# Kernel tuning notes

Measured on AMD Instinct MI355X. Metric: run time of the kernel, lower is better.

The kernel has to match this reference:

```python
import jax, jax.numpy as jnp
import numpy as np


def _pairwise_sqdist(a, b):
    # a: [m, n, d], b: [m, n, d] -> M: [m, n, n], M[m,i,j] = ||a[m,i]-b[m,j]||^2
    # Use the expansion |a|^2 + |b|^2 - 2 a.b to avoid materializing the
    # [m, n, n, d] difference tensor; clamp tiny negatives from cancellation.
    a2 = jnp.sum(a * a, axis=-1)  # [m, n]
    b2 = jnp.sum(b * b, axis=-1)  # [m, n]
    ab = jnp.einsum('mid,mjd->mij', a, b)  # [m, n, n]
    return jnp.maximum(a2[:, :, None] + b2[:, None, :] - 2.0 * ab, 0.0)


def setup_inputs() -> dict:
    key = jax.random.key(0)
    k1, k2 = jax.random.split(key)
    template = jax.random.normal(k1, (16, 4096, 3), dtype=jnp.float32)
    source = jax.random.normal(k2, (16, 4096, 3), dtype=jnp.float32)
    return {"template": template, "source": source}


def reference(template, source):
    M = _pairwise_sqdist(template, source)  # [m, n, n]
    # min over template index (axis 1): nearest template point for each source point
    dist1 = jnp.mean(jnp.sqrt(jnp.min(M, axis=1)))
    # min over source index (axis 2): nearest source point for each template point
    dist2 = jnp.mean(jnp.sqrt(jnp.min(M, axis=2)))
    return (dist1 + dist2) / 2.0
```

## Files before the change

### kernel.cpp

```cpp
#include <hip/hip_runtime.h>

#define N_PTS   4096
#define N_BATCH 16
#define INV_CNT (1.0f / (2.0f * N_BATCH * N_PTS))
#define AROW_BYTES ((size_t)2 * N_BATCH * N_PTS * 16 * 2)
#define NBLK    512

typedef _Float16 f16x8  __attribute__((ext_vector_type(8)));

__global__ __launch_bounds__(256) void prep_kernel(
    const float* __restrict__ tpl, const float* __restrict__ src,
    _Float16* __restrict__ arow, float* __restrict__ out) {
    int pt = blockIdx.x * 256 + threadIdx.x;
    if (pt == 0) out[0] = 0.0f;
    const float* p = (pt < 65536 ? tpl : src) + (size_t)(pt & 65535) * 3;
    float x = p[0], y = p[1], z = p[2];
    float o2 = fmaf(x, x, fmaf(y, y, z * z));
    _Float16 xh = (_Float16)x, yh = (_Float16)y, zh = (_Float16)z;
    _Float16 xl = (_Float16)(x - (float)xh);
    _Float16 yl = (_Float16)(y - (float)yh);
    _Float16 zl = (_Float16)(z - (float)zh);
    _Float16 o2h = (_Float16)o2;
    _Float16 o2l = (_Float16)(o2 - (float)o2h);
    const _Float16 m2 = (_Float16)-2.0f;
    f16x8 v0, v1;
    v0[0] = m2 * xh; v0[1] = m2 * yh; v0[2] = m2 * zh;
    v0[3] = m2 * xl; v0[4] = m2 * yl; v0[5] = m2 * zl;
    v0[6] = m2 * xh; v0[7] = m2 * yh;
    v1[0] = m2 * zh; v1[1] = o2h; v1[2] = o2l;
    v1[3] = (_Float16)0.0f; v1[4] = (_Float16)0.0f; v1[5] = (_Float16)0.0f;
    v1[6] = (_Float16)0.0f; v1[7] = (_Float16)0.0f;
    *(f16x8*)(arow + (size_t)pt * 16)     = v0;
    *(f16x8*)(arow + (size_t)pt * 16 + 8) = v1;
}

#define FD(a,x,y) "v_min3_f32 %[" #a "], v" #x ", v" #y ", %[" #a "]\n\t"
#define FOLD_D0A FD(acc0,32,33) FD(acc1,34,35) FD(acc0,36,37) FD(acc1,38,39) \
                 FD(acc0,40,41) FD(acc1,42,43) FD(acc0,44,45) FD(acc1,46,47)
#define FOLD_D0B FD(acc0,48,49) FD(acc1,50,51) FD(acc0,52,53) FD(acc1,54,55) \
                 FD(acc0,56,57) FD(acc1,58,59) FD(acc0,60,61) FD(acc1,62,63)
#define FOLD_D1A FD(acc2,64,65) FD(acc3,66,67) FD(acc2,68,69) FD(acc3,70,71) \
                 FD(acc2,72,73) FD(acc3,74,75) FD(acc2,76,77) FD(acc3,78,79)
#define FOLD_D1B FD(acc2,80,81) FD(acc3,82,83) FD(acc2,84,85) FD(acc3,86,87) \
                 FD(acc2,88,89) FD(acc3,90,91) FD(acc2,92,93) FD(acc3,94,95)
#define LD(s,off) "global_load_dwordx4 %[" #s "], %[voff], %[sb] offset:" #off "\n\t"
#define TILE_E(s,off) "s_waitcnt vmcnt(7)\n\t" \
  "v_mfma_f32_32x32x16_f16 v[32:47], %[" #s "], %[bf0], v[96:111]\n\t" \
  "v_mfma_f32_32x32x16_f16 v[64:79], %[" #s "], %[bf1], v[96:111]\n\t" \
  LD(s,off) FOLD_D0B FOLD_D1B
#define TILE_O(s,off) "s_waitcnt vmcnt(7)\n\t" \
  "v_mfma_f32_32x32x16_f16 v[48:63], %[" #s "], %[bf0], v[96:111]\n\t" \
  "v_mfma_f32_32x32x16_f16 v[80:95], %[" #s "], %[bf1], v[96:111]\n\t" \
  LD(s,off) FOLD_D0A FOLD_D1A
#define ZM(r)  "v_mov_b32 v" #r ", 0\n\t"
#define IM(r)  "v_mov_b32 v" #r ", 0x7f800000\n\t"

__global__ __launch_bounds__(256, 2) void chamfer_mfma(
    const float* __restrict__ tpl, const float* __restrict__ src,
    const _Float16* __restrict__ arow, float* __restrict__ blocksum,
    float* __restrict__ out) {
    __shared__ float wsum[4];

    const int tid = threadIdx.x;
    const int wv = tid >> 6, lane = tid & 63;
    const int n = lane & 31, g = lane >> 5;
    const int qb = blockIdx.x, batch = blockIdx.y, dir = blockIdx.z;

    const float* qpts = (dir == 0) ? src : tpl;
    const _Float16* abase = arow + ((dir == 0) ? (size_t)0 : (size_t)65536 * 16)
                          + (size_t)batch * 4096 * 16;

    f16x8 bfr[2];
    float p2[2];
    #pragma unroll
    for (int i = 0; i < 2; ++i) {
        const int q = qb * 256 + wv * 64 + i * 32 + n;
        const float* p = qpts + (size_t)(batch * 4096 + q) * 3;
        float px = p[0], py = p[1], pz = p[2];
        p2[i] = fmaf(px, px, fmaf(py, py, pz * pz));
        _Float16 xh = (_Float16)px, yh = (_Float16)py, zh = (_Float16)pz;
        _Float16 xl = (_Float16)(px - (float)xh);
        _Float16 yl = (_Float16)(py - (float)yh);
        _Float16 zl = (_Float16)(pz - (float)zh);
        f16x8 b;
        if (g == 0) {
            b[0] = xh; b[1] = yh; b[2] = zh;
            b[3] = xh; b[4] = yh; b[5] = zh;
            b[6] = xl; b[7] = yl;
        } else {
            b[0] = zl; b[1] = (_Float16)1.0f; b[2] = (_Float16)1.0f;
            b[3] = (_Float16)0.0f; b[4] = (_Float16)0.0f; b[5] = (_Float16)0.0f;
            b[6] = (_Float16)0.0f; b[7] = (_Float16)0.0f;
        }
        bfr[i] = b;
    }

    int voff = n * 32 + g * 16;
    int cnt = 16;
    float acc0 = 1e30f, acc1 = 1e30f, acc2 = 1e30f, acc3 = 1e30f;
    f16x8 r0, r1, r2, r3, r4, r5, r6, r7;

    asm volatile(
        ZM(96) ZM(97) ZM(98) ZM(99) ZM(100) ZM(101) ZM(102) ZM(103)
        ZM(104) ZM(105) ZM(106) ZM(107) ZM(108) ZM(109) ZM(110) ZM(111)
        IM(48) IM(49) IM(50) IM(51) IM(52) IM(53) IM(54) IM(55)
        IM(56) IM(57) IM(58) IM(59) IM(60) IM(61) IM(62) IM(63)
        IM(80) IM(81) IM(82) IM(83) IM(84) IM(85) IM(86) IM(87)
        IM(88) IM(89) IM(90) IM(91) IM(92) IM(93) IM(94) IM(95)
        LD(r0,0) LD(r1,1024) LD(r2,2048) LD(r3,3072)
        "v_add_u32 %[voff], 0x1000, %[voff]\n\t"
        LD(r4,0) LD(r5,1024) LD(r6,2048) LD(r7,3072)
        "v_add_u32 %[voff], 0x1000, %[voff]\n\t"
        "L_cham_%=:\n\t"
        TILE_E(r0,0) TILE_O(r1,1024) TILE_E(r2,2048) TILE_O(r3,3072)
        "v_add_u32 %[voff], 0x1000, %[voff]\n\t"
        TILE_E(r4,0) TILE_O(r5,1024) TILE_E(r6,2048) TILE_O(r7,3072)
        "v_add_u32 %[voff], 0x1000, %[voff]\n\t"
        "s_sub_u32 %[cnt], %[cnt], 1\n\t"
        "s_cmp_lg_u32 %[cnt], 0\n\t"
        "s_cbranch_scc1 L_cham_%=\n\t"
        "s_nop 7\n\t" "s_nop 7\n\t" "s_nop 7\n\t"
        FOLD_D0B FOLD_D1B
        "s_waitcnt vmcnt(0)\n\t"
        : [r0]"=&v"(r0), [r1]"=&v"(r1), [r2]"=&v"(r2), [r3]"=&v"(r3),
          [r4]"=&v"(r4), [r5]"=&v"(r5), [r6]"=&v"(r6), [r7]"=&v"(r7),
          [voff]"+v"(voff), [cnt]"+s"(cnt),
          [acc0]"+v"(acc0), [acc1]"+v"(acc1), [acc2]"+v"(acc2), [acc3]"+v"(acc3)
        : [bf0]"v"(bfr[0]), [bf1]"v"(bfr[1]), [sb]"s"(abase)
        : "memory", "scc",
          "v32","v33","v34","v35","v36","v37","v38","v39",
          "v40","v41","v42","v43","v44","v45","v46","v47",
          "v48","v49","v50","v51","v52","v53","v54","v55",
          "v56","v57","v58","v59","v60","v61","v62","v63",
          "v64","v65","v66","v67","v68","v69","v70","v71",
          "v72","v73","v74","v75","v76","v77","v78","v79",
          "v80","v81","v82","v83","v84","v85","v86","v87",
          "v88","v89","v90","v91","v92","v93","v94","v95",
          "v96","v97","v98","v99","v100","v101","v102","v103",
          "v104","v105","v106","v107","v108","v109","v110","v111");

    float v0 = fminf(acc0, acc1);
    v0 = fminf(v0, __shfl_xor(v0, 32));
    float v1 = fminf(acc2, acc3);
    v1 = fminf(v1, __shfl_xor(v1, 32));
    float d0 = fmaxf(v0 + p2[0], 0.0f);
    float d1 = fmaxf(v1 + p2[1], 0.0f);
    float s = (sqrtf(d0) + sqrtf(d1)) * INV_CNT;
    if (g != 0) s = 0.0f;
    #pragma unroll
    for (int off = 32; off > 0; off >>= 1) s += __shfl_down(s, off);
    if (lane == 0) wsum[wv] = s;
    __syncthreads();
    if (tid == 0) {
        float t = wsum[0] + wsum[1] + wsum[2] + wsum[3];
        if (blocksum) {
            int flat = (blockIdx.z * N_BATCH + blockIdx.y) * 16 + blockIdx.x;
            blocksum[flat] = t;
        } else {
            atomicAdd(out, t);
        }
    }
}

__global__ __launch_bounds__(256) void final_kernel(
    const float* __restrict__ blocksum, float* __restrict__ out) {
    __shared__ float wsum[4];
    float s = 0.0f;
    #pragma unroll
    for (int j = 0; j < NBLK / 256; ++j)
        s += blocksum[j * 256 + threadIdx.x];
    #pragma unroll
    for (int off = 32; off > 0; off >>= 1) s += __shfl_down(s, off);
    if ((threadIdx.x & 63) == 0) wsum[threadIdx.x >> 6] = s;
    __syncthreads();
    if (threadIdx.x == 0) out[0] = wsum[0] + wsum[1] + wsum[2] + wsum[3];
}

extern "C" void kernel_launch(void* const* d_in, const int* in_sizes, int n_in,
                              void* d_out, int out_size, void* d_ws, size_t ws_size,
                              hipStream_t stream) {
    const float* tpl = (const float*)d_in[0];
    const float* src = (const float*)d_in[1];
    float* out = (float*)d_out;
    _Float16* arow = (_Float16*)d_ws;
    const bool roomy = ws_size >= AROW_BYTES + 8192 + NBLK * sizeof(float);
    float* blocksum = roomy ? (float*)((char*)d_ws + AROW_BYTES + 8192) : nullptr;

    hipLaunchKernelGGL(prep_kernel, dim3((2 * N_BATCH * N_PTS) / 256),
                       dim3(256), 0, stream, tpl, src, arow, out);
    dim3 grid(N_PTS / 256, N_BATCH, 2);
    hipLaunchKernelGGL(chamfer_mfma, grid, dim3(256), 0, stream,
                       tpl, src, arow, blocksum, out);
    if (roomy)
        hipLaunchKernelGGL(final_kernel, dim3(1), dim3(256), 0, stream,
                           blocksum, out);
}
```

Before: 76.80 us.

## Give each wave four query tiles and split the key range across wave pairs

Each wave now holds four B-fragments (128 query points) instead of two, so every loaded A tile feeds four MFMAs rather than two. That halves the per-wave global loads per unit of compute. The key range is split between two wave halves (kh), each iterating half as many times, and the partial minima are combined through shared memory before the sqrt and sum. Register use grows substantially (accumulators up to v175), which may reduce occupancy below the launch-bounds target of two blocks per SIMD. The workspace slack is also enlarged so the loads that run past the end of the key range stay inside the buffer.

```diff
diff --git a/kernel.cpp b/kernel.cpp
--- a/kernel.cpp
+++ b/kernel.cpp
@@ -4,6 +4,7 @@
 #define N_BATCH 16
 #define INV_CNT (1.0f / (2.0f * N_BATCH * N_PTS))
 #define AROW_BYTES ((size_t)2 * N_BATCH * N_PTS * 16 * 2)
+#define SLACK   16384
 #define NBLK    512
 
 typedef _Float16 f16x8  __attribute__((ext_vector_type(8)));
@@ -35,23 +36,37 @@
 }
 
 #define FD(a,x,y) "v_min3_f32 %[" #a "], v" #x ", v" #y ", %[" #a "]\n\t"
-#define FOLD_D0A FD(acc0,32,33) FD(acc1,34,35) FD(acc0,36,37) FD(acc1,38,39) \
-                 FD(acc0,40,41) FD(acc1,42,43) FD(acc0,44,45) FD(acc1,46,47)
-#define FOLD_D0B FD(acc0,48,49) FD(acc1,50,51) FD(acc0,52,53) FD(acc1,54,55) \
-                 FD(acc0,56,57) FD(acc1,58,59) FD(acc0,60,61) FD(acc1,62,63)
-#define FOLD_D1A FD(acc2,64,65) FD(acc3,66,67) FD(acc2,68,69) FD(acc3,70,71) \
-                 FD(acc2,72,73) FD(acc3,74,75) FD(acc2,76,77) FD(acc3,78,79)
-#define FOLD_D1B FD(acc2,80,81) FD(acc3,82,83) FD(acc2,84,85) FD(acc3,86,87) \
-                 FD(acc2,88,89) FD(acc3,90,91) FD(acc2,92,93) FD(acc3,94,95)
+#define FOLD_A \
+  FD(acc0,32,33)  FD(acc1,34,35)  FD(acc0,36,37)  FD(acc1,38,39)  \
+  FD(acc0,40,41)  FD(acc1,42,43)  FD(acc0,44,45)  FD(acc1,46,47)  \
+  FD(acc2,48,49)  FD(acc3,50,51)  FD(acc2,52,53)  FD(acc3,54,55)  \
+  FD(acc2,56,57)  FD(acc3,58,59)  FD(acc2,60,61)  FD(acc3,62,63)  \
+  FD(acc4,64,65)  FD(acc5,66,67)  FD(acc4,68,69)  FD(acc5,70,71)  \
+  FD(acc4,72,73)  FD(acc5,74,75)  FD(acc4,76,77)  FD(acc5,78,79)  \
+  FD(acc6,80,81)  FD(acc7,82,83)  FD(acc6,84,85)  FD(acc7,86,87)  \
+  FD(acc6,88,89)  FD(acc7,90,91)  FD(acc6,92,93)  FD(acc7,94,95)
+#define FOLD_B \
+  FD(acc0,96,97)   FD(acc1,98,99)   FD(acc0,100,101) FD(acc1,102,103) \
+  FD(acc0,104,105) FD(acc1,106,107) FD(acc0,108,109) FD(acc1,110,111) \
+  FD(acc2,112,113) FD(acc3,114,115) FD(acc2,116,117) FD(acc3,118,119) \
+  FD(acc2,120,121) FD(acc3,122,123) FD(acc2,124,125) FD(acc3,126,127) \
+  FD(acc4,128,129) FD(acc5,130,131) FD(acc4,132,133) FD(acc5,134,135) \
+  FD(acc4,136,137) FD(acc5,138,139) FD(acc4,140,141) FD(acc5,142,143) \
+  FD(acc6,144,145) FD(acc7,146,147) FD(acc6,148,149) FD(acc7,150,151) \
+  FD(acc6,152,153) FD(acc7,154,155) FD(acc6,156,157) FD(acc7,158,159)
+#define MFA(s) \
+  "v_mfma_f32_32x32x16_f16 v[32:47], %["  #s "], %[bf0], v[160:175]\n\t" \
+  "v_mfma_f32_32x32x16_f16 v[48:63], %["  #s "], %[bf1], v[160:175]\n\t" \
+  "v_mfma_f32_32x32x16_f16 v[64:79], %["  #s "], %[bf2], v[160:175]\n\t" \
+  "v_mfma_f32_32x32x16_f16 v[80:95], %["  #s "], %[bf3], v[160:175]\n\t"
+#define MFB(s) \
+  "v_mfma_f32_32x32x16_f16 v[96:111],  %[" #s "], %[bf0], v[160:175]\n\t" \
+  "v_mfma_f32_32x32x16_f16 v[112:127], %[" #s "], %[bf1], v[160:175]\n\t" \
+  "v_mfma_f32_32x32x16_f16 v[128:143], %[" #s "], %[bf2], v[160:175]\n\t" \
+  "v_mfma_f32_32x32x16_f16 v[144:159], %[" #s "], %[bf3], v[160:175]\n\t"
 #define LD(s,off) "global_load_dwordx4 %[" #s "], %[voff], %[sb] offset:" #off "\n\t"
-#define TILE_E(s,off) "s_waitcnt vmcnt(7)\n\t" \
-  "v_mfma_f32_32x32x16_f16 v[32:47], %[" #s "], %[bf0], v[96:111]\n\t" \
-  "v_mfma_f32_32x32x16_f16 v[64:79], %[" #s "], %[bf1], v[96:111]\n\t" \
-  LD(s,off) FOLD_D0B FOLD_D1B
-#define TILE_O(s,off) "s_waitcnt vmcnt(7)\n\t" \
-  "v_mfma_f32_32x32x16_f16 v[48:63], %[" #s "], %[bf0], v[96:111]\n\t" \
-  "v_mfma_f32_32x32x16_f16 v[80:95], %[" #s "], %[bf1], v[96:111]\n\t" \
-  LD(s,off) FOLD_D0A FOLD_D1A
+#define TILE_E(s,off) "s_waitcnt vmcnt(7)\n\t" MFA(s) LD(s,off) FOLD_B
+#define TILE_O(s,off) "s_waitcnt vmcnt(7)\n\t" MFB(s) LD(s,off) FOLD_A
 #define ZM(r)  "v_mov_b32 v" #r ", 0\n\t"
 #define IM(r)  "v_mov_b32 v" #r ", 0x7f800000\n\t"
 
@@ -59,22 +74,24 @@
     const float* __restrict__ tpl, const float* __restrict__ src,
     const _Float16* __restrict__ arow, float* __restrict__ blocksum,
     float* __restrict__ out) {
+    __shared__ float cmb[2][2][4][32];
     __shared__ float wsum[4];
 
     const int tid = threadIdx.x;
     const int wv = tid >> 6, lane = tid & 63;
     const int n = lane & 31, g = lane >> 5;
+    const int qg = wv & 1, kh = wv >> 1;
     const int qb = blockIdx.x, batch = blockIdx.y, dir = blockIdx.z;
 
     const float* qpts = (dir == 0) ? src : tpl;
     const _Float16* abase = arow + ((dir == 0) ? (size_t)0 : (size_t)65536 * 16)
                           + (size_t)batch * 4096 * 16;
 
-    f16x8 bfr[2];
-    float p2[2];
-    #pragma unroll
-    for (int i = 0; i < 2; ++i) {
-        const int q = qb * 256 + wv * 64 + i * 32 + n;
+    f16x8 bfr[4];
+    float p2[4];
+    #pragma unroll
+    for (int i = 0; i < 4; ++i) {
+        const int q = qb * 256 + qg * 128 + i * 32 + n;
         const float* p = qpts + (size_t)(batch * 4096 + q) * 3;
         float px = p[0], py = p[1], pz = p[2];
         p2[i] = fmaf(px, px, fmaf(py, py, pz * pz));
@@ -95,18 +112,23 @@
         bfr[i] = b;
     }
 
-    int voff = n * 32 + g * 16;
-    int cnt = 16;
+    int voff = kh * 65536 + n * 32 + g * 16;
+    int cnt = 8;
     float acc0 = 1e30f, acc1 = 1e30f, acc2 = 1e30f, acc3 = 1e30f;
+    float acc4 = 1e30f, acc5 = 1e30f, acc6 = 1e30f, acc7 = 1e30f;
     f16x8 r0, r1, r2, r3, r4, r5, r6, r7;
 
     asm volatile(
-        ZM(96) ZM(97) ZM(98) ZM(99) ZM(100) ZM(101) ZM(102) ZM(103)
-        ZM(104) ZM(105) ZM(106) ZM(107) ZM(108) ZM(109) ZM(110) ZM(111)
-        IM(48) IM(49) IM(50) IM(51) IM(52) IM(53) IM(54) IM(55)
-        IM(56) IM(57) IM(58) IM(59) IM(60) IM(61) IM(62) IM(63)
-        IM(80) IM(81) IM(82) IM(83) IM(84) IM(85) IM(86) IM(87)
-        IM(88) IM(89) IM(90) IM(91) IM(92) IM(93) IM(94) IM(95)
+        ZM(160) ZM(161) ZM(162) ZM(163) ZM(164) ZM(165) ZM(166) ZM(167)
+        ZM(168) ZM(169) ZM(170) ZM(171) ZM(172) ZM(173) ZM(174) ZM(175)
+        IM(96)  IM(97)  IM(98)  IM(99)  IM(100) IM(101) IM(102) IM(103)
+        IM(104) IM(105) IM(106) IM(107) IM(108) IM(109) IM(110) IM(111)
+        IM(112) IM(113) IM(114) IM(115) IM(116) IM(117) IM(118) IM(119)
+        IM(120) IM(121) IM(122) IM(123) IM(124) IM(125) IM(126) IM(127)
+        IM(128) IM(129) IM(130) IM(131) IM(132) IM(133) IM(134) IM(135)
+        IM(136) IM(137) IM(138) IM(139) IM(140) IM(141) IM(142) IM(143)
+        IM(144) IM(145) IM(146) IM(147) IM(148) IM(149) IM(150) IM(151)
+        IM(152) IM(153) IM(154) IM(155) IM(156) IM(157) IM(158) IM(159)
         LD(r0,0) LD(r1,1024) LD(r2,2048) LD(r3,3072)
         "v_add_u32 %[voff], 0x1000, %[voff]\n\t"
         LD(r4,0) LD(r5,1024) LD(r6,2048) LD(r7,3072)
@@ -120,13 +142,15 @@
         "s_cmp_lg_u32 %[cnt], 0\n\t"
         "s_cbranch_scc1 L_cham_%=\n\t"
         "s_nop 7\n\t" "s_nop 7\n\t" "s_nop 7\n\t"
-        FOLD_D0B FOLD_D1B
+        FOLD_B
         "s_waitcnt vmcnt(0)\n\t"
         : [r0]"=&v"(r0), [r1]"=&v"(r1), [r2]"=&v"(r2), [r3]"=&v"(r3),
           [r4]"=&v"(r4), [r5]"=&v"(r5), [r6]"=&v"(r6), [r7]"=&v"(r7),
           [voff]"+v"(voff), [cnt]"+s"(cnt),
-          [acc0]"+v"(acc0), [acc1]"+v"(acc1), [acc2]"+v"(acc2), [acc3]"+v"(acc3)
-        : [bf0]"v"(bfr[0]), [bf1]"v"(bfr[1]), [sb]"s"(abase)
+          [acc0]"+v"(acc0), [acc1]"+v"(acc1), [acc2]"+v"(acc2), [acc3]"+v"(acc3),
+          [acc4]"+v"(acc4), [acc5]"+v"(acc5), [acc6]"+v"(acc6), [acc7]"+v"(acc7)
+        : [bf0]"v"(bfr[0]), [bf1]"v"(bfr[1]), [bf2]"v"(bfr[2]), [bf3]"v"(bfr[3]),
+          [sb]"s"(abase)
         : "memory", "scc",
           "v32","v33","v34","v35","v36","v37","v38","v39",
           "v40","v41","v42","v43","v44","v45","v46","v47",
@@ -137,16 +161,36 @@
           "v80","v81","v82","v83","v84","v85","v86","v87",
           "v88","v89","v90","v91","v92","v93","v94","v95",
           "v96","v97","v98","v99","v100","v101","v102","v103",
-          "v104","v105","v106","v107","v108","v109","v110","v111");
-
-    float v0 = fminf(acc0, acc1);
-    v0 = fminf(v0, __shfl_xor(v0, 32));
-    float v1 = fminf(acc2, acc3);
-    v1 = fminf(v1, __shfl_xor(v1, 32));
-    float d0 = fmaxf(v0 + p2[0], 0.0f);
-    float d1 = fmaxf(v1 + p2[1], 0.0f);
-    float s = (sqrtf(d0) + sqrtf(d1)) * INV_CNT;
-    if (g != 0) s = 0.0f;
+          "v104","v105","v106","v107","v108","v109","v110","v111",
+          "v112","v113","v114","v115","v116","v117","v118","v119",
+          "v120","v121","v122","v123","v124","v125","v126","v127",
+          "v128","v129","v130","v131","v132","v133","v134","v135",
+          "v136","v137","v138","v139","v140","v141","v142","v143",
+          "v144","v145","v146","v147","v148","v149","v150","v151",
+          "v152","v153","v154","v155","v156","v157","v158","v159",
+          "v160","v161","v162","v163","v164","v165","v166","v167",
+          "v168","v169","v170","v171","v172","v173","v174","v175");
+
+    #pragma unroll
+    for (int i = 0; i < 4; ++i) {
+        float v = fminf(i == 0 ? fminf(acc0, acc1) :
+                        i == 1 ? fminf(acc2, acc3) :
+                        i == 2 ? fminf(acc4, acc5) : fminf(acc6, acc7), 1e30f);
+        v = fminf(v, __shfl_xor(v, 32));
+        if (g == 0) cmb[qg][kh][i][n] = v;
+    }
+    __syncthreads();
+
+    float s = 0.0f;
+    if (kh == 0 && g == 0) {
+        #pragma unroll
+        for (int i = 0; i < 4; ++i) {
+            float m = fminf(cmb[qg][0][i][n], cmb[qg][1][i][n]);
+            float d = fmaxf(m + p2[i], 0.0f);
+            s += sqrtf(d);
+        }
+        s *= INV_CNT;
+    }
     #pragma unroll
     for (int off = 32; off > 0; off >>= 1) s += __shfl_down(s, off);
     if (lane == 0) wsum[wv] = s;
@@ -183,8 +227,8 @@
     const float* src = (const float*)d_in[1];
     float* out = (float*)d_out;
     _Float16* arow = (_Float16*)d_ws;
-    const bool roomy = ws_size >= AROW_BYTES + 8192 + NBLK * sizeof(float);
-    float* blocksum = roomy ? (float*)((char*)d_ws + AROW_BYTES + 8192) : nullptr;
+    const bool roomy = ws_size >= AROW_BYTES + SLACK + NBLK * sizeof(float);
+    float* blocksum = roomy ? (float*)((char*)d_ws + AROW_BYTES + SLACK) : nullptr;
 
     hipLaunchKernelGGL(prep_kernel, dim3((2 * N_BATCH * N_PTS) / 256),
                        dim3(256), 0, stream, tpl, src, arow, out);
```

New measurement: 79.79 us. +3.9%, slower.
